# Kernel tuning notes

Hardware: AMD Instinct MI355X
Metric: run time of the kernel (lower is better)

## Reference

```python
import jax, jax.numpy as jnp
import numpy as np

N_HEAD, M_DIM, K_DIM, V_DIM = 16, 1024, 64, 64
LN_EPS = 1e-5


def setup_inputs() -> dict:
    key = jax.random.key(0)
    ks = jax.random.split(key, 10)
    B, L = 4, 2048
    q = jax.random.normal(ks[0], (B, L, M_DIM), dtype=jnp.float32)
    k = jax.random.normal(ks[1], (B, L, M_DIM), dtype=jnp.float32)
    v = jax.random.normal(ks[2], (B, L, M_DIM), dtype=jnp.float32)
    s = 1.0 / np.sqrt(M_DIM)
    W_qs = jax.random.normal(ks[3], (M_DIM, N_HEAD * K_DIM), dtype=jnp.float32) * s
    W_ks = jax.random.normal(ks[4], (M_DIM, N_HEAD * K_DIM), dtype=jnp.float32) * s
    W_vs = jax.random.normal(ks[5], (M_DIM, N_HEAD * V_DIM), dtype=jnp.float32) * s
    fc_w = jax.random.normal(ks[6], (N_HEAD * V_DIM, M_DIM), dtype=jnp.float32) * (1.0 / np.sqrt(N_HEAD * V_DIM))
    fc_b = jnp.zeros((M_DIM,), dtype=jnp.float32)
    ln_g = jnp.ones((M_DIM,), dtype=jnp.float32)
    ln_b = jnp.zeros((M_DIM,), dtype=jnp.float32)
    return {"q": q, "k": k, "v": v, "W_qs": W_qs, "W_ks": W_ks, "W_vs": W_vs,
            "fc_w": fc_w, "fc_b": fc_b, "ln_g": ln_g, "ln_b": ln_b}


def reference(q, k, v, W_qs, W_ks, W_vs, fc_w, fc_b, ln_g, ln_b):
    B, Lq, _ = q.shape
    residual = q
    # project and split heads: [B, L, H, D]
    qh = (q @ W_qs).reshape(B, Lq, N_HEAD, K_DIM)
    kh = (k @ W_ks).reshape(B, k.shape[1], N_HEAD, K_DIM)
    vh = (v @ W_vs).reshape(B, v.shape[1], N_HEAD, V_DIM)
    temperature = np.power(K_DIM, 0.5).astype(np.float32)
    # attention scores [B, H, Lq, Lk]
    attn = jnp.einsum('bqhd,bkhd->bhqk', qh, kh) / temperature
    attn = jax.nn.softmax(attn, axis=-1)
    out = jnp.einsum('bhqk,bkhd->bqhd', attn, vh).reshape(B, Lq, N_HEAD * V_DIM)
    out = out @ fc_w + fc_b
    x = out + residual
    mu = jnp.mean(x, axis=-1, keepdims=True)
    var = jnp.mean(jnp.square(x - mu), axis=-1, keepdims=True)
    return (x - mu) * jax.lax.rsqrt(var + LN_EPS) * ln_g + ln_b
```

## Files before the change

kernel.cpp:

```cpp
#include <hip/hip_runtime.h>
#include <math.h>

#define NHEAD 16
#define MDIM  1024
#define KD    64
#define BATCH 4
#define SEQ   2048
#define MROWS (BATCH*SEQ)

using short8 = __attribute__((ext_vector_type(8))) short;
using f4     = __attribute__((ext_vector_type(4))) float;
using f16x   = __attribute__((ext_vector_type(16))) float;

__device__ inline short f2bf(float x) {
  union { float f; unsigned u; } v; v.f = x;
  unsigned r = v.u + 0x7fffu + ((v.u >> 16) & 1u);
  return (short)(r >> 16);
}

__device__ __forceinline__ float fast_exp2(float x) {
#if __has_builtin(__builtin_amdgcn_exp2f)
  return __builtin_amdgcn_exp2f(x);
#else
  return exp2f(x);
#endif
}

__device__ __forceinline__ int pack_bf16(float lo, float hi) {
#if __has_builtin(__builtin_amdgcn_cvt_pk_bf16_f32)
  auto t = __builtin_amdgcn_cvt_pk_bf16_f32(lo, hi);
  int r; __builtin_memcpy(&r, &t, 4); return r;
#else
  unsigned u0 = __float_as_uint(lo) + 0x8000u;
  unsigned u1 = __float_as_uint(hi) + 0x8000u;
  return (int)__builtin_amdgcn_perm(u1, u0, 0x07060302u);
#endif
}

__device__ __forceinline__ void g2l16(const void* g, void* l) {
  __builtin_amdgcn_global_load_lds((const __attribute__((address_space(1))) unsigned int*)g,
                                   (__attribute__((address_space(3))) unsigned int*)l, 16, 0, 0);
}

#define AHIP_WAIT_LGKM0 asm volatile("s_waitcnt lgkmcnt(0)" ::: "memory")
#define AHIP_WAIT_VM6   asm volatile("s_waitcnt vmcnt(6)" ::: "memory")
#define AHIP_WAIT_VM0   asm volatile("s_waitcnt vmcnt(0)" ::: "memory")
#define AHIP_SFENCE     __builtin_amdgcn_sched_barrier(0)
#define AHIP_BAR        __builtin_amdgcn_s_barrier()

__global__ void wtrans_kernel(const float* __restrict__ w0, const float* __restrict__ w1,
                              const float* __restrict__ w2, const float* __restrict__ w3,
                              short* __restrict__ o0, short* __restrict__ o1,
                              short* __restrict__ o2, short* __restrict__ o3) {
  int z = blockIdx.z;
  const float* in = z == 0 ? w0 : (z == 1 ? w1 : (z == 2 ? w2 : w3));
  short* out = z == 0 ? o0 : (z == 1 ? o1 : (z == 2 ? o2 : o3));
  __shared__ float t[32][33];
  int bx = blockIdx.x * 32, by = blockIdx.y * 32;
  int tx = threadIdx.x, ty = threadIdx.y;
#pragma unroll
  for (int i = 0; i < 4; i++)
    t[ty + i * 8][tx] = in[(size_t)(by + ty + i * 8) * MDIM + bx + tx];
  __syncthreads();
#pragma unroll
  for (int i = 0; i < 4; i++)
    out[(size_t)(bx + ty + i * 8) * MDIM + by + tx] = f2bf(t[tx][ty + i * 8]);
}

__global__ void cvt_kernel(const float* __restrict__ q, const float* __restrict__ k,
                           const float* __restrict__ v, short* __restrict__ qb,
                           short* __restrict__ kb, short* __restrict__ vb) {
  const float* in = blockIdx.y == 0 ? q : (blockIdx.y == 1 ? k : v);
  short* out = blockIdx.y == 0 ? qb : (blockIdx.y == 1 ? kb : vb);
  size_t i = (size_t)blockIdx.x * 256 + threadIdx.x;
  float4 a = ((const float4*)in)[2 * i];
  float4 b = ((const float4*)in)[2 * i + 1];
  short8 s = {f2bf(a.x), f2bf(a.y), f2bf(a.z), f2bf(a.w),
              f2bf(b.x), f2bf(b.y), f2bf(b.z), f2bf(b.w)};
  ((short8*)out)[i] = s;
}

#define G8_PROLOGUE(Ab, Bt)                                                            \
  int tid = threadIdx.x, wid = tid >> 6, lane = tid & 63;                              \
  int quad = lane >> 4, low = lane & 15;                                               \
  int l8 = lane & 7, lr = lane >> 3;                                                   \
  int wrow = (wid >> 2) * 128, wcol = (wid & 3) * 32;                                  \
  const short* aS = Ab + (size_t)(m0 + wid * 32 + lr) * 1024 + (l8 ^ lr) * 8;          \
  const short* bS = Bt + (size_t)(n0 + wid * 16 + lr) * 1024 + (l8 ^ lr) * 8;          \
  auto stage = [&](int t, int b) {                                                     \
    const short* a = aS + t * 64;                                                      \
    const short* bb = bS + t * 64;                                                     \
    short* ad = &As[b][wid * 2048];                                                    \
    short* bd = &Bs[b][wid * 1024];                                                    \
    g2l16(a, ad);                                                                      \
    g2l16(a + 8 * 1024, ad + 512);                                                     \
    g2l16(a + 16 * 1024, ad + 1024);                                                   \
    g2l16(a + 24 * 1024, ad + 1536);                                                   \
    g2l16(bb, bd);                                                                     \
    g2l16(bb + 8 * 1024, bd + 512);                                                    \
  };                                                                                   \
  f4 acc[8][2];                                                                        \
  _Pragma("unroll")                                                                    \
  for (int mf = 0; mf < 8; mf++)                                                       \
    _Pragma("unroll")                                                                  \
    for (int nf = 0; nf < 2; nf++) {                                                   \
      acc[mf][nf][0] = 0.f; acc[mf][nf][1] = 0.f;                                      \
      acc[mf][nf][2] = 0.f; acc[mf][nf][3] = 0.f;                                      \
    }                                                                                  \
  stage(0, 0);                                                                         \
  stage(1, 1);                                                                         \
  AHIP_WAIT_VM6; AHIP_SFENCE; AHIP_BAR; AHIP_SFENCE;

#define G8_MAIN_LOOP()                                                                 \
  for (int t = 0; t < 16; ++t) {                                                       \
    const int cur = t & 1;                                                             \
    short8 af[2][8], bfv[2][2];                                                        \
    _Pragma("unroll")                                                                  \
    for (int kk = 0; kk < 2; kk++) {                                                   \
      _Pragma("unroll")                                                                \
      for (int mf = 0; mf < 8; mf++)                                                   \
        af[kk][mf] = *(const short8*)&As[cur][(wrow + mf * 16 + low) * 64 +            \
                                              (((kk * 4 + quad) ^ (low & 7)) * 8)];    \
      _Pragma("unroll")                                                                \
      for (int nf = 0; nf < 2; nf++)                                                   \
        bfv[kk][nf] = *(const short8*)&Bs[cur][(wcol + nf * 16 + low) * 64 +           \
                                               (((kk * 4 + quad) ^ (low & 7)) * 8)];   \
    }                                                                                  \
    AHIP_WAIT_LGKM0; AHIP_SFENCE;                                                      \
    AHIP_BAR; AHIP_SFENCE;                                                             \
    if (t + 2 < 16) stage(t + 2, cur);                                                 \
    __builtin_amdgcn_s_setprio(1);                                                     \
    _Pragma("unroll")                                                                  \
    for (int kk = 0; kk < 2; kk++)                                                     \
      _Pragma("unroll")                                                                \
      for (int mf = 0; mf < 8; mf++)                                                   \
        _Pragma("unroll")                                                              \
        for (int nf = 0; nf < 2; nf++)                                                 \
          acc[mf][nf] = __builtin_amdgcn_mfma_f32_16x16x32_bf16(af[kk][mf],            \
                          bfv[kk][nf], acc[mf][nf], 0, 0, 0);                          \
    __builtin_amdgcn_s_setprio(0);                                                     \
    AHIP_SFENCE;                                                                       \
    if (t + 2 < 16) { AHIP_WAIT_VM6; } else { AHIP_WAIT_VM0; }                         \
    AHIP_SFENCE; AHIP_BAR; AHIP_SFENCE;                                                \
  }

__launch_bounds__(512, 2)
__global__ void gemm_qkv_kernel(const short* __restrict__ qb, const short* __restrict__ kb,
                                const short* __restrict__ vb, const short* __restrict__ Wqt,
                                const short* __restrict__ Wkt, const short* __restrict__ Wvt,
                                short* __restrict__ Qh, short* __restrict__ Kh,
                                short* __restrict__ Vt) {
  __shared__ __attribute__((aligned(16))) short As[2][256 * 64];
  __shared__ __attribute__((aligned(16))) short Bs[2][128 * 64];
  int z = blockIdx.z;
  const short* Ab = z == 0 ? qb : (z == 1 ? kb : vb);
  const short* Bt = z == 0 ? Wqt : (z == 1 ? Wkt : Wvt);
  int m0 = blockIdx.x * 256, n0 = blockIdx.y * 128;

  G8_PROLOGUE(Ab, Bt)
  G8_MAIN_LOOP()

  float scale = z == 0 ? 0.18033688011112042f : 1.0f;
  short* dst = z == 0 ? Qh : (z == 1 ? Kh : Vt);
#pragma unroll
  for (int mf = 0; mf < 8; mf++)
#pragma unroll
    for (int nf = 0; nf < 2; nf++)
#pragma unroll
      for (int r2 = 0; r2 < 4; r2++) {
        int gr = m0 + wrow + mf * 16 + quad * 4 + r2;
        int gc = n0 + wcol + nf * 16 + low;
        float val = acc[mf][nf][r2];
        int b = gr >> 11, l = gr & 2047, h = gc >> 6, d = gc & 63;
        if (z < 2)
          dst[(((size_t)(b * NHEAD + h)) * SEQ + l) * KD + d] = f2bf(val * scale);
        else
          dst[(((size_t)(b * NHEAD + h)) * KD + d) * SEQ + l] = f2bf(val);
      }
}

__launch_bounds__(512, 2)
__global__ void gemm_fc_kernel(const short* __restrict__ Ab, const short* __restrict__ Bt,
                               float* __restrict__ dst, const float* __restrict__ bias,
                               const float* __restrict__ res) {
  __shared__ __attribute__((aligned(16))) short As[2][256 * 64];
  __shared__ __attribute__((aligned(16))) short Bs[2][128 * 64];
  int m0 = blockIdx.x * 256, n0 = blockIdx.y * 128;

  G8_PROLOGUE(Ab, Bt)
  G8_MAIN_LOOP()

#pragma unroll
  for (int mf = 0; mf < 8; mf++)
#pragma unroll
    for (int nf = 0; nf < 2; nf++)
#pragma unroll
      for (int r2 = 0; r2 < 4; r2++) {
        int gr = m0 + wrow + mf * 16 + quad * 4 + r2;
        int gc = n0 + wcol + nf * 16 + low;
        dst[(size_t)gr * 1024 + gc] = acc[mf][nf][r2] + bias[gc] + res[(size_t)gr * 1024 + gc];
      }
}

__launch_bounds__(256, 4)
__global__ void attn_kernel(const short* __restrict__ Qh, const short* __restrict__ Kh,
                            const short* __restrict__ Vt, short* __restrict__ Out) {
  __shared__ __attribute__((aligned(16))) short KT[2][64 * 64];
  __shared__ __attribute__((aligned(16))) short VT[2][64 * 64];
  int tid = threadIdx.x;
  int wave = tid >> 6, lane = tid & 63;
  int l = lane & 31, hi = lane >> 5;
  int bh = blockIdx.y;
  int q0 = blockIdx.x * 128 + wave * 32;

  const short* Qb = Qh + (size_t)bh * SEQ * KD;
  const short* Kb = Kh + (size_t)bh * SEQ * KD;
  const short* Vb = Vt + (size_t)bh * KD * SEQ;

  int srow = lane >> 3;
  int sch = (lane & 7) ^ srow;
  const short* kSrc0 = Kb + (size_t)(wave * 16 + srow) * KD + sch * 8;
  const short* kSrc1 = kSrc0 + (size_t)8 * KD;
  const short* vSrc0 = Vb + (size_t)(wave * 16 + srow) * SEQ + sch * 8;
  const short* vSrc1 = vSrc0 + (size_t)8 * SEQ;

  auto stage = [&](int k0, int b) {
    g2l16(kSrc0 + (size_t)k0 * KD, &KT[b][wave * 1024]);
    g2l16(kSrc1 + (size_t)k0 * KD, &KT[b][wave * 1024 + 512]);
    g2l16(vSrc0 + k0, &VT[b][wave * 1024]);
    g2l16(vSrc1 + k0, &VT[b][wave * 1024 + 512]);
  };

  short8 qf[4];
#pragma unroll
  for (int ks = 0; ks < 4; ks++)
    qf[ks] = *(const short8*)&Qb[(size_t)(q0 + l) * KD + ks * 16 + hi * 8];

  f16x Oacc[2], lacc;
#pragma unroll
  for (int i = 0; i < 16; i++) { Oacc[0][i] = 0.f; Oacc[1][i] = 0.f; lacc[i] = 0.f; }
  const short8 onesb = {0x3F80, 0x3F80, 0x3F80, 0x3F80, 0x3F80, 0x3F80, 0x3F80, 0x3F80};

  stage(0, 0);
  __syncthreads();

  for (int c = 0; c < SEQ / 64; c++) {
    int b = c & 1;
    if (c + 1 < SEQ / 64) stage((c + 1) * 64, b ^ 1);

#pragma unroll
    for (int nt = 0; nt < 2; nt++) {
      short8 kf[4];
#pragma unroll
      for (int ks = 0; ks < 4; ks++)
        kf[ks] = *(const short8*)&KT[b][(nt * 32 + l) * 64 + (((ks * 2 + hi) ^ (l & 7)) * 8)];

      f16x S;
#pragma unroll
      for (int i = 0; i < 16; i++) S[i] = 0.f;
      __builtin_amdgcn_s_setprio(1);
#pragma unroll
      for (int ks = 0; ks < 4; ks++)
        S = __builtin_amdgcn_mfma_f32_32x32x16_bf16(kf[ks], qf[ks], S, 0, 0, 0);
      __builtin_amdgcn_s_setprio(0);

      int u[8];
#pragma unroll
      for (int i = 0; i < 8; i++)
        u[i] = pack_bf16(fast_exp2(S[2 * i]), fast_exp2(S[2 * i + 1]));
      asm("v_permlane32_swap_b32 %0, %1" : "+v"(u[0]), "+v"(u[2]));
      asm("v_permlane32_swap_b32 %0, %1" : "+v"(u[1]), "+v"(u[3]));
      asm("v_permlane32_swap_b32 %0, %1" : "+v"(u[4]), "+v"(u[6]));
      asm("v_permlane32_swap_b32 %0, %1" : "+v"(u[5]), "+v"(u[7]));
      short8 pa0, pa1;
      {
        int t0[4] = {u[0], u[1], u[2], u[3]};
        int t1[4] = {u[4], u[5], u[6], u[7]};
        __builtin_memcpy(&pa0, t0, 16);
        __builtin_memcpy(&pa1, t1, 16);
      }

      __builtin_amdgcn_s_setprio(1);
      lacc = __builtin_amdgcn_mfma_f32_32x32x16_bf16(pa0, onesb, lacc, 0, 0, 0);
      lacc = __builtin_amdgcn_mfma_f32_32x32x16_bf16(pa1, onesb, lacc, 0, 0, 0);

#pragma unroll
      for (int dt = 0; dt < 2; dt++) {
        short8 vf0 = *(const short8*)&VT[b][(dt * 32 + l) * 64 + (((nt * 4 + 0 + hi) ^ (l & 7)) * 8)];
        short8 vf1 = *(const short8*)&VT[b][(dt * 32 + l) * 64 + (((nt * 4 + 2 + hi) ^ (l & 7)) * 8)];
        Oacc[dt] = __builtin_amdgcn_mfma_f32_32x32x16_bf16(pa0, vf0, Oacc[dt], 0, 0, 0);
        Oacc[dt] = __builtin_amdgcn_mfma_f32_32x32x16_bf16(pa1, vf1, Oacc[dt], 0, 0, 0);
      }
      __builtin_amdgcn_s_setprio(0);
    }
    __syncthreads();
  }

  int bb = bh >> 4, h = bh & 15;
#pragma unroll
  for (int r = 0; r < 16; r++) {
    int qrow = q0 + (r & 3) + 8 * (r >> 2) + 4 * hi;
    float iv = 1.0f / lacc[r];
#pragma unroll
    for (int dt = 0; dt < 2; dt++) {
      size_t idx = ((size_t)(bb * SEQ + qrow)) * 1024 + h * 64 + dt * 32 + l;
      Out[idx] = f2bf(Oacc[dt][r] * iv);
    }
  }
}

__launch_bounds__(256)
__global__ void ln_kernel(const float* __restrict__ x, const float* __restrict__ g,
                          const float* __restrict__ b, float* __restrict__ out) {
  int row = blockIdx.x, tid = threadIdx.x;
  const float4* xr = (const float4*)(x + (size_t)row * 1024);
  float4 v = xr[tid];
  float s = v.x + v.y + v.z + v.w;
  float q = v.x * v.x + v.y * v.y + v.z * v.z + v.w * v.w;
#pragma unroll
  for (int o = 32; o > 0; o >>= 1) { s += __shfl_xor(s, o); q += __shfl_xor(q, o); }
  __shared__ float ss[4], sq[4];
  if ((tid & 63) == 0) { ss[tid >> 6] = s; sq[tid >> 6] = q; }
  __syncthreads();
  if (tid == 0) {
    float S = ss[0] + ss[1] + ss[2] + ss[3];
    float Q = sq[0] + sq[1] + sq[2] + sq[3];
    float mean = S * (1.f / 1024.f);
    float var = Q * (1.f / 1024.f) - mean * mean;
    ss[0] = mean; sq[0] = rsqrtf(var + 1e-5f);
  }
  __syncthreads();
  float mean = ss[0], rs = sq[0];
  const float4* g4 = (const float4*)g;
  const float4* b4 = (const float4*)b;
  float4 gg = g4[tid], bb = b4[tid], o;
  o.x = (v.x - mean) * rs * gg.x + bb.x;
  o.y = (v.y - mean) * rs * gg.y + bb.y;
  o.z = (v.z - mean) * rs * gg.z + bb.z;
  o.w = (v.w - mean) * rs * gg.w + bb.w;
  ((float4*)(out + (size_t)row * 1024))[tid] = o;
}

extern "C" void kernel_launch(void* const* d_in, const int* in_sizes, int n_in,
                              void* d_out, int out_size, void* d_ws, size_t ws_size,
                              hipStream_t stream) {
  const float* q   = (const float*)d_in[0];
  const float* k   = (const float*)d_in[1];
  const float* v   = (const float*)d_in[2];
  const float* Wq  = (const float*)d_in[3];
  const float* Wk  = (const float*)d_in[4];
  const float* Wv  = (const float*)d_in[5];
  const float* fcw = (const float*)d_in[6];
  const float* fcb = (const float*)d_in[7];
  const float* lng = (const float*)d_in[8];
  const float* lnb = (const float*)d_in[9];
  float* out = (float*)d_out;

  char* ws = (char*)d_ws;
  const size_t MB = 1024 * 1024;
  short* Wqt = (short*)(ws + 0 * MB);
  short* Wkt = (short*)(ws + 2 * MB);
  short* Wvt = (short*)(ws + 4 * MB);
  short* fct = (short*)(ws + 6 * MB);
  short* qb  = (short*)(ws + 8 * MB);
  short* kb  = (short*)(ws + 24 * MB);
  short* vb  = (short*)(ws + 40 * MB);
  short* Kh  = (short*)(ws + 8 * MB);
  short* Vt  = (short*)(ws + 24 * MB);
  short* Ao  = (short*)(ws + 40 * MB);
  short* Qh  = (short*)(ws + 56 * MB);
  float* X   = (float*)(ws + 8 * MB);

  wtrans_kernel<<<dim3(32, 32, 4), dim3(32, 8), 0, stream>>>(Wq, Wk, Wv, fcw, Wqt, Wkt, Wvt, fct);

  cvt_kernel<<<dim3(MROWS * MDIM / 8 / 256, 3), 256, 0, stream>>>(q, k, v, qb, kb, vb);

  gemm_qkv_kernel<<<dim3(32, 8, 3), 512, 0, stream>>>(qb, kb, vb, Wqt, Wkt, Wvt, Qh, Kh, Vt);

  attn_kernel<<<dim3(SEQ / 128, BATCH * NHEAD), 256, 0, stream>>>(Qh, Kh, Vt, Ao);

  gemm_fc_kernel<<<dim3(32, 8), 512, 0, stream>>>(Ao, fct, X, fcb, q);

  ln_kernel<<<MROWS, 256, 0, stream>>>(X, lng, lnb, out);
}
```

Before: 360.6 us.

## Halve GEMM M-tile to 128 rows and restructure attention inner loop

The QKV and FC GEMMs now use 128x128 tiles instead of 256x128, which doubles the grid and lets launch bounds target 4 blocks per CU with half the A-tile LDS. The aim is better occupancy and load balance across CUs, at the cost of less A/B reuse per block and more global traffic. The attention kernel's two-subtile loop is manually unrolled so both QK^T score MFMAs are issued before the exp and PV work. This gives the scheduler more independent MFMA and VALU work to overlap, but raises register pressure.

Measured after the change: 348.5 us. 3.4% less time.

```diff
diff --git a/kernel.cpp b/kernel.cpp
--- a/kernel.cpp
+++ b/kernel.cpp
@@ -43,7 +43,7 @@
 }
 
 #define AHIP_WAIT_LGKM0 asm volatile("s_waitcnt lgkmcnt(0)" ::: "memory")
-#define AHIP_WAIT_VM6   asm volatile("s_waitcnt vmcnt(6)" ::: "memory")
+#define AHIP_WAIT_VM4   asm volatile("s_waitcnt vmcnt(4)" ::: "memory")
 #define AHIP_WAIT_VM0   asm volatile("s_waitcnt vmcnt(0)" ::: "memory")
 #define AHIP_SFENCE     __builtin_amdgcn_sched_barrier(0)
 #define AHIP_BAR        __builtin_amdgcn_s_barrier()
@@ -84,24 +84,22 @@
   int tid = threadIdx.x, wid = tid >> 6, lane = tid & 63;                              \
   int quad = lane >> 4, low = lane & 15;                                               \
   int l8 = lane & 7, lr = lane >> 3;                                                   \
-  int wrow = (wid >> 2) * 128, wcol = (wid & 3) * 32;                                  \
-  const short* aS = Ab + (size_t)(m0 + wid * 32 + lr) * 1024 + (l8 ^ lr) * 8;          \
+  int wrow = (wid >> 2) * 64, wcol = (wid & 3) * 32;                                   \
+  const short* aS = Ab + (size_t)(m0 + wid * 16 + lr) * 1024 + (l8 ^ lr) * 8;          \
   const short* bS = Bt + (size_t)(n0 + wid * 16 + lr) * 1024 + (l8 ^ lr) * 8;          \
   auto stage = [&](int t, int b) {                                                     \
     const short* a = aS + t * 64;                                                      \
     const short* bb = bS + t * 64;                                                     \
-    short* ad = &As[b][wid * 2048];                                                    \
+    short* ad = &As[b][wid * 1024];                                                    \
     short* bd = &Bs[b][wid * 1024];                                                    \
     g2l16(a, ad);                                                                      \
     g2l16(a + 8 * 1024, ad + 512);                                                     \
-    g2l16(a + 16 * 1024, ad + 1024);                                                   \
-    g2l16(a + 24 * 1024, ad + 1536);                                                   \
     g2l16(bb, bd);                                                                     \
     g2l16(bb + 8 * 1024, bd + 512);                                                    \
   };                                                                                   \
-  f4 acc[8][2];                                                                        \
+  f4 acc[4][2];                                                                        \
   _Pragma("unroll")                                                                    \
-  for (int mf = 0; mf < 8; mf++)                                                       \
+  for (int mf = 0; mf < 4; mf++)                                                       \
     _Pragma("unroll")                                                                  \
     for (int nf = 0; nf < 2; nf++) {                                                   \
       acc[mf][nf][0] = 0.f; acc[mf][nf][1] = 0.f;                                      \
@@ -109,16 +107,16 @@
     }                                                                                  \
   stage(0, 0);                                                                         \
   stage(1, 1);                                                                         \
-  AHIP_WAIT_VM6; AHIP_SFENCE; AHIP_BAR; AHIP_SFENCE;
+  AHIP_WAIT_VM4; AHIP_SFENCE; AHIP_BAR; AHIP_SFENCE;
 
 #define G8_MAIN_LOOP()                                                                 \
   for (int t = 0; t < 16; ++t) {                                                       \
     const int cur = t & 1;                                                             \
-    short8 af[2][8], bfv[2][2];                                                        \
+    short8 af[2][4], bfv[2][2];                                                        \
     _Pragma("unroll")                                                                  \
     for (int kk = 0; kk < 2; kk++) {                                                   \
       _Pragma("unroll")                                                                \
-      for (int mf = 0; mf < 8; mf++)                                                   \
+      for (int mf = 0; mf < 4; mf++)                                                   \
         af[kk][mf] = *(const short8*)&As[cur][(wrow + mf * 16 + low) * 64 +            \
                                               (((kk * 4 + quad) ^ (low & 7)) * 8)];    \
       _Pragma("unroll")                                                                \
@@ -133,29 +131,29 @@
     _Pragma("unroll")                                                                  \
     for (int kk = 0; kk < 2; kk++)                                                     \
       _Pragma("unroll")                                                                \
-      for (int mf = 0; mf < 8; mf++)                                                   \
+      for (int mf = 0; mf < 4; mf++)                                                   \
         _Pragma("unroll")                                                              \
         for (int nf = 0; nf < 2; nf++)                                                 \
           acc[mf][nf] = __builtin_amdgcn_mfma_f32_16x16x32_bf16(af[kk][mf],            \
                           bfv[kk][nf], acc[mf][nf], 0, 0, 0);                          \
     __builtin_amdgcn_s_setprio(0);                                                     \
     AHIP_SFENCE;                                                                       \
-    if (t + 2 < 16) { AHIP_WAIT_VM6; } else { AHIP_WAIT_VM0; }                         \
+    if (t + 2 < 16) { AHIP_WAIT_VM4; } else { AHIP_WAIT_VM0; }                         \
     AHIP_SFENCE; AHIP_BAR; AHIP_SFENCE;                                                \
   }
 
-__launch_bounds__(512, 2)
+__launch_bounds__(512, 4)
 __global__ void gemm_qkv_kernel(const short* __restrict__ qb, const short* __restrict__ kb,
                                 const short* __restrict__ vb, const short* __restrict__ Wqt,
                                 const short* __restrict__ Wkt, const short* __restrict__ Wvt,
                                 short* __restrict__ Qh, short* __restrict__ Kh,
                                 short* __restrict__ Vt) {
-  __shared__ __attribute__((aligned(16))) short As[2][256 * 64];
+  __shared__ __attribute__((aligned(16))) short As[2][128 * 64];
   __shared__ __attribute__((aligned(16))) short Bs[2][128 * 64];
   int z = blockIdx.z;
   const short* Ab = z == 0 ? qb : (z == 1 ? kb : vb);
   const short* Bt = z == 0 ? Wqt : (z == 1 ? Wkt : Wvt);
-  int m0 = blockIdx.x * 256, n0 = blockIdx.y * 128;
+  int m0 = blockIdx.x * 128, n0 = blockIdx.y * 128;
 
   G8_PROLOGUE(Ab, Bt)
   G8_MAIN_LOOP()
@@ -163,7 +161,7 @@
   float scale = z == 0 ? 0.18033688011112042f : 1.0f;
   short* dst = z == 0 ? Qh : (z == 1 ? Kh : Vt);
 #pragma unroll
-  for (int mf = 0; mf < 8; mf++)
+  for (int mf = 0; mf < 4; mf++)
 #pragma unroll
     for (int nf = 0; nf < 2; nf++)
 #pragma unroll
@@ -179,19 +177,19 @@
       }
 }
 
-__launch_bounds__(512, 2)
+__launch_bounds__(512, 4)
 __global__ void gemm_fc_kernel(const short* __restrict__ Ab, const short* __restrict__ Bt,
                                float* __restrict__ dst, const float* __restrict__ bias,
                                const float* __restrict__ res) {
-  __shared__ __attribute__((aligned(16))) short As[2][256 * 64];
+  __shared__ __attribute__((aligned(16))) short As[2][128 * 64];
   __shared__ __attribute__((aligned(16))) short Bs[2][128 * 64];
-  int m0 = blockIdx.x * 256, n0 = blockIdx.y * 128;
+  int m0 = blockIdx.x * 128, n0 = blockIdx.y * 128;
 
   G8_PROLOGUE(Ab, Bt)
   G8_MAIN_LOOP()
 
 #pragma unroll
-  for (int mf = 0; mf < 8; mf++)
+  for (int mf = 0; mf < 4; mf++)
 #pragma unroll
     for (int nf = 0; nf < 2; nf++)
 #pragma unroll
@@ -248,49 +246,97 @@
     int b = c & 1;
     if (c + 1 < SEQ / 64) stage((c + 1) * 64, b ^ 1);
 
-#pragma unroll
-    for (int nt = 0; nt < 2; nt++) {
-      short8 kf[4];
+    f16x S0, S1;
+    {
+      short8 kf0[4];
 #pragma unroll
       for (int ks = 0; ks < 4; ks++)
-        kf[ks] = *(const short8*)&KT[b][(nt * 32 + l) * 64 + (((ks * 2 + hi) ^ (l & 7)) * 8)];
-
-      f16x S;
-#pragma unroll
-      for (int i = 0; i < 16; i++) S[i] = 0.f;
+        kf0[ks] = *(const short8*)&KT[b][l * 64 + (((ks * 2 + hi) ^ (l & 7)) * 8)];
+      f16x z;
+#pragma unroll
+      for (int i = 0; i < 16; i++) z[i] = 0.f;
       __builtin_amdgcn_s_setprio(1);
+      S0 = __builtin_amdgcn_mfma_f32_32x32x16_bf16(kf0[0], qf[0], z, 0, 0, 0);
+      S0 = __builtin_amdgcn_mfma_f32_32x32x16_bf16(kf0[1], qf[1], S0, 0, 0, 0);
+      S0 = __builtin_amdgcn_mfma_f32_32x32x16_bf16(kf0[2], qf[2], S0, 0, 0, 0);
+      S0 = __builtin_amdgcn_mfma_f32_32x32x16_bf16(kf0[3], qf[3], S0, 0, 0, 0);
+      __builtin_amdgcn_s_setprio(0);
+    }
+    {
+      short8 kf1[4];
 #pragma unroll
       for (int ks = 0; ks < 4; ks++)
-        S = __builtin_amdgcn_mfma_f32_32x32x16_bf16(kf[ks], qf[ks], S, 0, 0, 0);
+        kf1[ks] = *(const short8*)&KT[b][(32 + l) * 64 + (((ks * 2 + hi) ^ (l & 7)) * 8)];
+      f16x z;
+#pragma unroll
+      for (int i = 0; i < 16; i++) z[i] = 0.f;
+      __builtin_amdgcn_s_setprio(1);
+      S1 = __builtin_amdgcn_mfma_f32_32x32x16_bf16(kf1[0], qf[0], z, 0, 0, 0);
+      S1 = __builtin_amdgcn_mfma_f32_32x32x16_bf16(kf1[1], qf[1], S1, 0, 0, 0);
+      S1 = __builtin_amdgcn_mfma_f32_32x32x16_bf16(kf1[2], qf[2], S1, 0, 0, 0);
+      S1 = __builtin_amdgcn_mfma_f32_32x32x16_bf16(kf1[3], qf[3], S1, 0, 0, 0);
       __builtin_amdgcn_s_setprio(0);
-
+    }
+
+    short8 pa00, pa01;
+    {
       int u[8];
 #pragma unroll
       for (int i = 0; i < 8; i++)
-        u[i] = pack_bf16(fast_exp2(S[2 * i]), fast_exp2(S[2 * i + 1]));
+        u[i] = pack_bf16(fast_exp2(S0[2 * i]), fast_exp2(S0[2 * i + 1]));
       asm("v_permlane32_swap_b32 %0, %1" : "+v"(u[0]), "+v"(u[2]));
       asm("v_permlane32_swap_b32 %0, %1" : "+v"(u[1]), "+v"(u[3]));
       asm("v_permlane32_swap_b32 %0, %1" : "+v"(u[4]), "+v"(u[6]));
       asm("v_permlane32_swap_b32 %0, %1" : "+v"(u[5]), "+v"(u[7]));
-      short8 pa0, pa1;
-      {
-        int t0[4] = {u[0], u[1], u[2], u[3]};
-        int t1[4] = {u[4], u[5], u[6], u[7]};
-        __builtin_memcpy(&pa0, t0, 16);
-        __builtin_memcpy(&pa1, t1, 16);
-      }
-
+      int t0[4] = {u[0], u[1], u[2], u[3]};
+      int t1[4] = {u[4], u[5], u[6], u[7]};
+      __builtin_memcpy(&pa00, t0, 16);
+      __builtin_memcpy(&pa01, t1, 16);
+    }
+
+    {
+      short8 vf00 = *(const short8*)&VT[b][l * 64 + (((0 + hi) ^ (l & 7)) * 8)];
+      short8 vf01 = *(const short8*)&VT[b][l * 64 + (((2 + hi) ^ (l & 7)) * 8)];
+      short8 vf10 = *(const short8*)&VT[b][(32 + l) * 64 + (((0 + hi) ^ (l & 7)) * 8)];
+      short8 vf11 = *(const short8*)&VT[b][(32 + l) * 64 + (((2 + hi) ^ (l & 7)) * 8)];
       __builtin_amdgcn_s_setprio(1);
-      lacc = __builtin_amdgcn_mfma_f32_32x32x16_bf16(pa0, onesb, lacc, 0, 0, 0);
-      lacc = __builtin_amdgcn_mfma_f32_32x32x16_bf16(pa1, onesb, lacc, 0, 0, 0);
-
-#pragma unroll
-      for (int dt = 0; dt < 2; dt++) {
-        short8 vf0 = *(const short8*)&VT[b][(dt * 32 + l) * 64 + (((nt * 4 + 0 + hi) ^ (l & 7)) * 8)];
-        short8 vf1 = *(const short8*)&VT[b][(dt * 32 + l) * 64 + (((nt * 4 + 2 + hi) ^ (l & 7)) * 8)];
-        Oacc[dt] = __builtin_amdgcn_mfma_f32_32x32x16_bf16(pa0, vf0, Oacc[dt], 0, 0, 0);
-        Oacc[dt] = __builtin_amdgcn_mfma_f32_32x32x16_bf16(pa1, vf1, Oacc[dt], 0, 0, 0);
-      }
+      lacc = __builtin_amdgcn_mfma_f32_32x32x16_bf16(pa00, onesb, lacc, 0, 0, 0);
+      lacc = __builtin_amdgcn_mfma_f32_32x32x16_bf16(pa01, onesb, lacc, 0, 0, 0);
+      Oacc[0] = __builtin_amdgcn_mfma_f32_32x32x16_bf16(pa00, vf00, Oacc[0], 0, 0, 0);
+      Oacc[0] = __builtin_amdgcn_mfma_f32_32x32x16_bf16(pa01, vf01, Oacc[0], 0, 0, 0);
+      Oacc[1] = __builtin_amdgcn_mfma_f32_32x32x16_bf16(pa00, vf10, Oacc[1], 0, 0, 0);
+      Oacc[1] = __builtin_amdgcn_mfma_f32_32x32x16_bf16(pa01, vf11, Oacc[1], 0, 0, 0);
+      __builtin_amdgcn_s_setprio(0);
+    }
+
+    short8 pa10, pa11;
+    {
+      int u[8];
+#pragma unroll
+      for (int i = 0; i < 8; i++)
+        u[i] = pack_bf16(fast_exp2(S1[2 * i]), fast_exp2(S1[2 * i + 1]));
+      asm("v_permlane32_swap_b32 %0, %1" : "+v"(u[0]), "+v"(u[2]));
+      asm("v_permlane32_swap_b32 %0, %1" : "+v"(u[1]), "+v"(u[3]));
+      asm("v_permlane32_swap_b32 %0, %1" : "+v"(u[4]), "+v"(u[6]));
+      asm("v_permlane32_swap_b32 %0, %1" : "+v"(u[5]), "+v"(u[7]));
+      int t0[4] = {u[0], u[1], u[2], u[3]};
+      int t1[4] = {u[4], u[5], u[6], u[7]};
+      __builtin_memcpy(&pa10, t0, 16);
+      __builtin_memcpy(&pa11, t1, 16);
+    }
+
+    {
+      short8 vf00 = *(const short8*)&VT[b][l * 64 + (((4 + hi) ^ (l & 7)) * 8)];
+      short8 vf01 = *(const short8*)&VT[b][l * 64 + (((6 + hi) ^ (l & 7)) * 8)];
+      short8 vf10 = *(const short8*)&VT[b][(32 + l) * 64 + (((4 + hi) ^ (l & 7)) * 8)];
+      short8 vf11 = *(const short8*)&VT[b][(32 + l) * 64 + (((6 + hi) ^ (l & 7)) * 8)];
+      __builtin_amdgcn_s_setprio(1);
+      lacc = __builtin_amdgcn_mfma_f32_32x32x16_bf16(pa10, onesb, lacc, 0, 0, 0);
+      lacc = __builtin_amdgcn_mfma_f32_32x32x16_bf16(pa11, onesb, lacc, 0, 0, 0);
+      Oacc[0] = __builtin_amdgcn_mfma_f32_32x32x16_bf16(pa10, vf00, Oacc[0], 0, 0, 0);
+      Oacc[0] = __builtin_amdgcn_mfma_f32_32x32x16_bf16(pa11, vf01, Oacc[0], 0, 0, 0);
+      Oacc[1] = __builtin_amdgcn_mfma_f32_32x32x16_bf16(pa10, vf10, Oacc[1], 0, 0, 0);
+      Oacc[1] = __builtin_amdgcn_mfma_f32_32x32x16_bf16(pa11, vf11, Oacc[1], 0, 0, 0);
       __builtin_amdgcn_s_setprio(0);
     }
     __syncthreads();
@@ -375,11 +421,11 @@
 
   cvt_kernel<<<dim3(MROWS * MDIM / 8 / 256, 3), 256, 0, stream>>>(q, k, v, qb, kb, vb);
 
-  gemm_qkv_kernel<<<dim3(32, 8, 3), 512, 0, stream>>>(qb, kb, vb, Wqt, Wkt, Wvt, Qh, Kh, Vt);
+  gemm_qkv_kernel<<<dim3(64, 8, 3), 512, 0, stream>>>(qb, kb, vb, Wqt, Wkt, Wvt, Qh, Kh, Vt);
 
   attn_kernel<<<dim3(SEQ / 128, BATCH * NHEAD), 256, 0, stream>>>(Qh, Kh, Vt, Ao);
 
-  gemm_fc_kernel<<<dim3(32, 8), 512, 0, stream>>>(Ao, fct, X, fcb, q);
+  gemm_fc_kernel<<<dim3(64, 8), 512, 0, stream>>>(Ao, fct, X, fcb, q);
 
   ln_kernel<<<MROWS, 256, 0, stream>>>(X, lng, lnb, out);
 }
```

## Halve GEMM M-tile and give attention waves two query tiles each

Applied to the files above, without the earlier changes.

The QKV and FC GEMMs move from 256x128 to 128x128 block tiles. That doubles the grid, and launch bounds now request four blocks per CU with smaller LDS buffers, so more work is resident per CU. The attention kernel drops to two waves per block, and each wave handles 64 query rows as two 32-row tiles. Each K/V fragment loaded from LDS is then reused across both query tiles, halving LDS reads per MFMA, at the cost of more accumulator registers per wave and fewer waves per block for latency hiding.

Measured after the change: 348.1 us. 1.04x faster.

```diff
diff --git a/kernel.cpp b/kernel.cpp
--- a/kernel.cpp
+++ b/kernel.cpp
@@ -43,7 +43,7 @@
 }
 
 #define AHIP_WAIT_LGKM0 asm volatile("s_waitcnt lgkmcnt(0)" ::: "memory")
-#define AHIP_WAIT_VM6   asm volatile("s_waitcnt vmcnt(6)" ::: "memory")
+#define AHIP_WAIT_VM4   asm volatile("s_waitcnt vmcnt(4)" ::: "memory")
 #define AHIP_WAIT_VM0   asm volatile("s_waitcnt vmcnt(0)" ::: "memory")
 #define AHIP_SFENCE     __builtin_amdgcn_sched_barrier(0)
 #define AHIP_BAR        __builtin_amdgcn_s_barrier()
@@ -84,24 +84,22 @@
   int tid = threadIdx.x, wid = tid >> 6, lane = tid & 63;                              \
   int quad = lane >> 4, low = lane & 15;                                               \
   int l8 = lane & 7, lr = lane >> 3;                                                   \
-  int wrow = (wid >> 2) * 128, wcol = (wid & 3) * 32;                                  \
-  const short* aS = Ab + (size_t)(m0 + wid * 32 + lr) * 1024 + (l8 ^ lr) * 8;          \
+  int wrow = (wid >> 2) * 64, wcol = (wid & 3) * 32;                                   \
+  const short* aS = Ab + (size_t)(m0 + wid * 16 + lr) * 1024 + (l8 ^ lr) * 8;          \
   const short* bS = Bt + (size_t)(n0 + wid * 16 + lr) * 1024 + (l8 ^ lr) * 8;          \
   auto stage = [&](int t, int b) {                                                     \
     const short* a = aS + t * 64;                                                      \
     const short* bb = bS + t * 64;                                                     \
-    short* ad = &As[b][wid * 2048];                                                    \
+    short* ad = &As[b][wid * 1024];                                                    \
     short* bd = &Bs[b][wid * 1024];                                                    \
     g2l16(a, ad);                                                                      \
     g2l16(a + 8 * 1024, ad + 512);                                                     \
-    g2l16(a + 16 * 1024, ad + 1024);                                                   \
-    g2l16(a + 24 * 1024, ad + 1536);                                                   \
     g2l16(bb, bd);                                                                     \
     g2l16(bb + 8 * 1024, bd + 512);                                                    \
   };                                                                                   \
-  f4 acc[8][2];                                                                        \
+  f4 acc[4][2];                                                                        \
   _Pragma("unroll")                                                                    \
-  for (int mf = 0; mf < 8; mf++)                                                       \
+  for (int mf = 0; mf < 4; mf++)                                                       \
     _Pragma("unroll")                                                                  \
     for (int nf = 0; nf < 2; nf++) {                                                   \
       acc[mf][nf][0] = 0.f; acc[mf][nf][1] = 0.f;                                      \
@@ -109,16 +107,16 @@
     }                                                                                  \
   stage(0, 0);                                                                         \
   stage(1, 1);                                                                         \
-  AHIP_WAIT_VM6; AHIP_SFENCE; AHIP_BAR; AHIP_SFENCE;
+  AHIP_WAIT_VM4; AHIP_SFENCE; AHIP_BAR; AHIP_SFENCE;
 
 #define G8_MAIN_LOOP()                                                                 \
   for (int t = 0; t < 16; ++t) {                                                       \
     const int cur = t & 1;                                                             \
-    short8 af[2][8], bfv[2][2];                                                        \
+    short8 af[2][4], bfv[2][2];                                                        \
     _Pragma("unroll")                                                                  \
     for (int kk = 0; kk < 2; kk++) {                                                   \
       _Pragma("unroll")                                                                \
-      for (int mf = 0; mf < 8; mf++)                                                   \
+      for (int mf = 0; mf < 4; mf++)                                                   \
         af[kk][mf] = *(const short8*)&As[cur][(wrow + mf * 16 + low) * 64 +            \
                                               (((kk * 4 + quad) ^ (low & 7)) * 8)];    \
       _Pragma("unroll")                                                                \
@@ -133,29 +131,29 @@
     _Pragma("unroll")                                                                  \
     for (int kk = 0; kk < 2; kk++)                                                     \
       _Pragma("unroll")                                                                \
-      for (int mf = 0; mf < 8; mf++)                                                   \
+      for (int mf = 0; mf < 4; mf++)                                                   \
         _Pragma("unroll")                                                              \
         for (int nf = 0; nf < 2; nf++)                                                 \
           acc[mf][nf] = __builtin_amdgcn_mfma_f32_16x16x32_bf16(af[kk][mf],            \
                           bfv[kk][nf], acc[mf][nf], 0, 0, 0);                          \
     __builtin_amdgcn_s_setprio(0);                                                     \
     AHIP_SFENCE;                                                                       \
-    if (t + 2 < 16) { AHIP_WAIT_VM6; } else { AHIP_WAIT_VM0; }                         \
+    if (t + 2 < 16) { AHIP_WAIT_VM4; } else { AHIP_WAIT_VM0; }                         \
     AHIP_SFENCE; AHIP_BAR; AHIP_SFENCE;                                                \
   }
 
-__launch_bounds__(512, 2)
+__launch_bounds__(512, 4)
 __global__ void gemm_qkv_kernel(const short* __restrict__ qb, const short* __restrict__ kb,
                                 const short* __restrict__ vb, const short* __restrict__ Wqt,
                                 const short* __restrict__ Wkt, const short* __restrict__ Wvt,
                                 short* __restrict__ Qh, short* __restrict__ Kh,
                                 short* __restrict__ Vt) {
-  __shared__ __attribute__((aligned(16))) short As[2][256 * 64];
+  __shared__ __attribute__((aligned(16))) short As[2][128 * 64];
   __shared__ __attribute__((aligned(16))) short Bs[2][128 * 64];
   int z = blockIdx.z;
   const short* Ab = z == 0 ? qb : (z == 1 ? kb : vb);
   const short* Bt = z == 0 ? Wqt : (z == 1 ? Wkt : Wvt);
-  int m0 = blockIdx.x * 256, n0 = blockIdx.y * 128;
+  int m0 = blockIdx.x * 128, n0 = blockIdx.y * 128;
 
   G8_PROLOGUE(Ab, Bt)
   G8_MAIN_LOOP()
@@ -163,7 +161,7 @@
   float scale = z == 0 ? 0.18033688011112042f : 1.0f;
   short* dst = z == 0 ? Qh : (z == 1 ? Kh : Vt);
 #pragma unroll
-  for (int mf = 0; mf < 8; mf++)
+  for (int mf = 0; mf < 4; mf++)
 #pragma unroll
     for (int nf = 0; nf < 2; nf++)
 #pragma unroll
@@ -179,19 +177,19 @@
       }
 }
 
-__launch_bounds__(512, 2)
+__launch_bounds__(512, 4)
 __global__ void gemm_fc_kernel(const short* __restrict__ Ab, const short* __restrict__ Bt,
                                float* __restrict__ dst, const float* __restrict__ bias,
                                const float* __restrict__ res) {
-  __shared__ __attribute__((aligned(16))) short As[2][256 * 64];
+  __shared__ __attribute__((aligned(16))) short As[2][128 * 64];
   __shared__ __attribute__((aligned(16))) short Bs[2][128 * 64];
-  int m0 = blockIdx.x * 256, n0 = blockIdx.y * 128;
+  int m0 = blockIdx.x * 128, n0 = blockIdx.y * 128;
 
   G8_PROLOGUE(Ab, Bt)
   G8_MAIN_LOOP()
 
 #pragma unroll
-  for (int mf = 0; mf < 8; mf++)
+  for (int mf = 0; mf < 4; mf++)
 #pragma unroll
     for (int nf = 0; nf < 2; nf++)
 #pragma unroll
@@ -202,7 +200,7 @@
       }
 }
 
-__launch_bounds__(256, 4)
+__launch_bounds__(128, 2)
 __global__ void attn_kernel(const short* __restrict__ Qh, const short* __restrict__ Kh,
                             const short* __restrict__ Vt, short* __restrict__ Out) {
   __shared__ __attribute__((aligned(16))) short KT[2][64 * 64];
@@ -211,7 +209,7 @@
   int wave = tid >> 6, lane = tid & 63;
   int l = lane & 31, hi = lane >> 5;
   int bh = blockIdx.y;
-  int q0 = blockIdx.x * 128 + wave * 32;
+  int q0 = blockIdx.x * 128 + wave * 64;
 
   const short* Qb = Qh + (size_t)bh * SEQ * KD;
   const short* Kb = Kh + (size_t)bh * SEQ * KD;
@@ -219,26 +217,36 @@
 
   int srow = lane >> 3;
   int sch = (lane & 7) ^ srow;
-  const short* kSrc0 = Kb + (size_t)(wave * 16 + srow) * KD + sch * 8;
-  const short* kSrc1 = kSrc0 + (size_t)8 * KD;
-  const short* vSrc0 = Vb + (size_t)(wave * 16 + srow) * SEQ + sch * 8;
-  const short* vSrc1 = vSrc0 + (size_t)8 * SEQ;
+  const short* kS = Kb + (size_t)(wave * 32 + srow) * KD + sch * 8;
+  const short* vS = Vb + (size_t)(wave * 32 + srow) * SEQ + sch * 8;
 
   auto stage = [&](int k0, int b) {
-    g2l16(kSrc0 + (size_t)k0 * KD, &KT[b][wave * 1024]);
-    g2l16(kSrc1 + (size_t)k0 * KD, &KT[b][wave * 1024 + 512]);
-    g2l16(vSrc0 + k0, &VT[b][wave * 1024]);
-    g2l16(vSrc1 + k0, &VT[b][wave * 1024 + 512]);
+    short* kd = &KT[b][wave * 2048];
+    short* vd = &VT[b][wave * 2048];
+#pragma unroll
+    for (int i = 0; i < 4; i++) {
+      g2l16(kS + (size_t)(k0 + i * 8) * KD, kd + i * 512);
+      g2l16(vS + (size_t)(i * 8) * SEQ + k0, vd + i * 512);
+    }
   };
 
-  short8 qf[4];
-#pragma unroll
-  for (int ks = 0; ks < 4; ks++)
-    qf[ks] = *(const short8*)&Qb[(size_t)(q0 + l) * KD + ks * 16 + hi * 8];
-
-  f16x Oacc[2], lacc;
-#pragma unroll
-  for (int i = 0; i < 16; i++) { Oacc[0][i] = 0.f; Oacc[1][i] = 0.f; lacc[i] = 0.f; }
+  short8 qf[2][4];
+#pragma unroll
+  for (int qt = 0; qt < 2; qt++)
+#pragma unroll
+    for (int ks = 0; ks < 4; ks++)
+      qf[qt][ks] = *(const short8*)&Qb[(size_t)(q0 + qt * 32 + l) * KD + ks * 16 + hi * 8];
+
+  f16x Oacc[2][2], lacc[2];
+#pragma unroll
+  for (int i = 0; i < 16; i++) {
+    Oacc[0][0][i] = 0.f; Oacc[0][1][i] = 0.f;
+    Oacc[1][0][i] = 0.f; Oacc[1][1][i] = 0.f;
+    lacc[0][i] = 0.f; lacc[1][i] = 0.f;
+  }
+  f16x fz;
+#pragma unroll
+  for (int i = 0; i < 16; i++) fz[i] = 0.f;
   const short8 onesb = {0x3F80, 0x3F80, 0x3F80, 0x3F80, 0x3F80, 0x3F80, 0x3F80, 0x3F80};
 
   stage(0, 0);
@@ -254,59 +262,63 @@
 #pragma unroll
       for (int ks = 0; ks < 4; ks++)
         kf[ks] = *(const short8*)&KT[b][(nt * 32 + l) * 64 + (((ks * 2 + hi) ^ (l & 7)) * 8)];
-
-      f16x S;
-#pragma unroll
-      for (int i = 0; i < 16; i++) S[i] = 0.f;
-      __builtin_amdgcn_s_setprio(1);
-#pragma unroll
-      for (int ks = 0; ks < 4; ks++)
-        S = __builtin_amdgcn_mfma_f32_32x32x16_bf16(kf[ks], qf[ks], S, 0, 0, 0);
-      __builtin_amdgcn_s_setprio(0);
-
-      int u[8];
-#pragma unroll
-      for (int i = 0; i < 8; i++)
-        u[i] = pack_bf16(fast_exp2(S[2 * i]), fast_exp2(S[2 * i + 1]));
-      asm("v_permlane32_swap_b32 %0, %1" : "+v"(u[0]), "+v"(u[2]));
-      asm("v_permlane32_swap_b32 %0, %1" : "+v"(u[1]), "+v"(u[3]));
-      asm("v_permlane32_swap_b32 %0, %1" : "+v"(u[4]), "+v"(u[6]));
-      asm("v_permlane32_swap_b32 %0, %1" : "+v"(u[5]), "+v"(u[7]));
-      short8 pa0, pa1;
-      {
-        int t0[4] = {u[0], u[1], u[2], u[3]};
-        int t1[4] = {u[4], u[5], u[6], u[7]};
-        __builtin_memcpy(&pa0, t0, 16);
-        __builtin_memcpy(&pa1, t1, 16);
+      short8 vf00 = *(const short8*)&VT[b][l * 64 + (((nt * 4 + 0 + hi) ^ (l & 7)) * 8)];
+      short8 vf01 = *(const short8*)&VT[b][l * 64 + (((nt * 4 + 2 + hi) ^ (l & 7)) * 8)];
+      short8 vf10 = *(const short8*)&VT[b][(32 + l) * 64 + (((nt * 4 + 0 + hi) ^ (l & 7)) * 8)];
+      short8 vf11 = *(const short8*)&VT[b][(32 + l) * 64 + (((nt * 4 + 2 + hi) ^ (l & 7)) * 8)];
+
+#pragma unroll
+      for (int qt = 0; qt < 2; qt++) {
+        f16x S;
+        __builtin_amdgcn_s_setprio(1);
+        S = __builtin_amdgcn_mfma_f32_32x32x16_bf16(kf[0], qf[qt][0], fz, 0, 0, 0);
+        S = __builtin_amdgcn_mfma_f32_32x32x16_bf16(kf[1], qf[qt][1], S, 0, 0, 0);
+        S = __builtin_amdgcn_mfma_f32_32x32x16_bf16(kf[2], qf[qt][2], S, 0, 0, 0);
+        S = __builtin_amdgcn_mfma_f32_32x32x16_bf16(kf[3], qf[qt][3], S, 0, 0, 0);
+        __builtin_amdgcn_s_setprio(0);
+
+        int u[8];
+#pragma unroll
+        for (int i = 0; i < 8; i++)
+          u[i] = pack_bf16(fast_exp2(S[2 * i]), fast_exp2(S[2 * i + 1]));
+        asm("v_permlane32_swap_b32 %0, %1" : "+v"(u[0]), "+v"(u[2]));
+        asm("v_permlane32_swap_b32 %0, %1" : "+v"(u[1]), "+v"(u[3]));
+        asm("v_permlane32_swap_b32 %0, %1" : "+v"(u[4]), "+v"(u[6]));
+        asm("v_permlane32_swap_b32 %0, %1" : "+v"(u[5]), "+v"(u[7]));
+        short8 pa0, pa1;
+        {
+          int t0[4] = {u[0], u[1], u[2], u[3]};
+          int t1[4] = {u[4], u[5], u[6], u[7]};
+          __builtin_memcpy(&pa0, t0, 16);
+          __builtin_memcpy(&pa1, t1, 16);
+        }
+
+        __builtin_amdgcn_s_setprio(1);
+        lacc[qt] = __builtin_amdgcn_mfma_f32_32x32x16_bf16(pa0, onesb, lacc[qt], 0, 0, 0);
+        lacc[qt] = __builtin_amdgcn_mfma_f32_32x32x16_bf16(pa1, onesb, lacc[qt], 0, 0, 0);
+        Oacc[qt][0] = __builtin_amdgcn_mfma_f32_32x32x16_bf16(pa0, vf00, Oacc[qt][0], 0, 0, 0);
+        Oacc[qt][0] = __builtin_amdgcn_mfma_f32_32x32x16_bf16(pa1, vf01, Oacc[qt][0], 0, 0, 0);
+        Oacc[qt][1] = __builtin_amdgcn_mfma_f32_32x32x16_bf16(pa0, vf10, Oacc[qt][1], 0, 0, 0);
+        Oacc[qt][1] = __builtin_amdgcn_mfma_f32_32x32x16_bf16(pa1, vf11, Oacc[qt][1], 0, 0, 0);
+        __builtin_amdgcn_s_setprio(0);
       }
-
-      __builtin_amdgcn_s_setprio(1);
-      lacc = __builtin_amdgcn_mfma_f32_32x32x16_bf16(pa0, onesb, lacc, 0, 0, 0);
-      lacc = __builtin_amdgcn_mfma_f32_32x32x16_bf16(pa1, onesb, lacc, 0, 0, 0);
-
-#pragma unroll
-      for (int dt = 0; dt < 2; dt++) {
-        short8 vf0 = *(const short8*)&VT[b][(dt * 32 + l) * 64 + (((nt * 4 + 0 + hi) ^ (l & 7)) * 8)];
-        short8 vf1 = *(const short8*)&VT[b][(dt * 32 + l) * 64 + (((nt * 4 + 2 + hi) ^ (l & 7)) * 8)];
-        Oacc[dt] = __builtin_amdgcn_mfma_f32_32x32x16_bf16(pa0, vf0, Oacc[dt], 0, 0, 0);
-        Oacc[dt] = __builtin_amdgcn_mfma_f32_32x32x16_bf16(pa1, vf1, Oacc[dt], 0, 0, 0);
-      }
-      __builtin_amdgcn_s_setprio(0);
     }
     __syncthreads();
   }
 
   int bb = bh >> 4, h = bh & 15;
 #pragma unroll
-  for (int r = 0; r < 16; r++) {
-    int qrow = q0 + (r & 3) + 8 * (r >> 2) + 4 * hi;
-    float iv = 1.0f / lacc[r];
-#pragma unroll
-    for (int dt = 0; dt < 2; dt++) {
-      size_t idx = ((size_t)(bb * SEQ + qrow)) * 1024 + h * 64 + dt * 32 + l;
-      Out[idx] = f2bf(Oacc[dt][r] * iv);
+  for (int qt = 0; qt < 2; qt++)
+#pragma unroll
+    for (int r = 0; r < 16; r++) {
+      int qrow = q0 + qt * 32 + (r & 3) + 8 * (r >> 2) + 4 * hi;
+      float iv = 1.0f / lacc[qt][r];
+#pragma unroll
+      for (int dt = 0; dt < 2; dt++) {
+        size_t idx = ((size_t)(bb * SEQ + qrow)) * 1024 + h * 64 + dt * 32 + l;
+        Out[idx] = f2bf(Oacc[qt][dt][r] * iv);
+      }
     }
-  }
 }
 
 __launch_bounds__(256)
@@ -375,11 +387,11 @@
 
   cvt_kernel<<<dim3(MROWS * MDIM / 8 / 256, 3), 256, 0, stream>>>(q, k, v, qb, kb, vb);
 
-  gemm_qkv_kernel<<<dim3(32, 8, 3), 512, 0, stream>>>(qb, kb, vb, Wqt, Wkt, Wvt, Qh, Kh, Vt);
-
-  attn_kernel<<<dim3(SEQ / 128, BATCH * NHEAD), 256, 0, stream>>>(Qh, Kh, Vt, Ao);
-
-  gemm_fc_kernel<<<dim3(32, 8), 512, 0, stream>>>(Ao, fct, X, fcb, q);
+  gemm_qkv_kernel<<<dim3(64, 8, 3), 512, 0, stream>>>(qb, kb, vb, Wqt, Wkt, Wvt, Qh, Kh, Vt);
+
+  attn_kernel<<<dim3(SEQ / 128, BATCH * NHEAD), 128, 0, stream>>>(Qh, Kh, Vt, Ao);
+
+  gemm_fc_kernel<<<dim3(64, 8), 512, 0, stream>>>(Ao, fct, X, fcb, q);
 
   ln_kernel<<<MROWS, 256, 0, stream>>>(X, lng, lnb, out);
 }
```
